# Kernel tuning notes

Measured on AMD Instinct MI355X. Metric: run time of the kernel, lower is better.

The kernel has to match this reference:

```python
import jax, jax.numpy as jnp
import numpy as np

N, C, H, K = 100000, 64, 8, 16
D = C // H  # head_dim = 8


def setup_inputs() -> dict:
    key = jax.random.key(0)
    ks = jax.random.split(key, 7)
    s = 1.0 / np.sqrt(C)
    return {
        "feats": jax.random.normal(ks[0], (N, C), jnp.float32),
        "knn_idx": jax.random.randint(ks[1], (N, K), 0, N, jnp.int32),
        "Wq": jax.random.normal(ks[2], (C, C), jnp.float32) * s,
        "Wk": jax.random.normal(ks[3], (C, C), jnp.float32) * s,
        "Wv": jax.random.normal(ks[4], (C, C), jnp.float32) * s,
        "Wo": jax.random.normal(ks[5], (C, C), jnp.float32) * s,
        "bo": jnp.zeros((C,), jnp.float32),
    }


def reference(feats, knn_idx, Wq, Wk, Wv, Wo, bo):
    # Projections (torch Linear y = x @ W^T expressed with pre-transposed W)
    q = (feats @ Wq).reshape(N, H, D)          # [N,H,D]
    k_feat = (feats @ Wk).reshape(N, H, D)     # [N,H,D]
    v = (feats @ Wv).reshape(N, H, D)          # [N,H,D]

    # Gather k-NN neighbors: [N,K,H,D]
    k_nb = k_feat[knn_idx]
    v_nb = v[knn_idx]

    # Scores: dot(q, k_neighbor) per head, scaled
    scores = jnp.einsum("nhd,nkhd->nkh", q, k_nb) / np.sqrt(D).astype(np.float32)
    attn = jax.nn.softmax(scores, axis=1)      # softmax over K neighbors

    out = jnp.einsum("nkh,nkhd->nhd", attn, v_nb).reshape(N, C)
    return out @ Wo + bo
```

## Files before the change

### kernel.cpp

```cpp
#include <hip/hip_runtime.h>
#include <hip/hip_fp16.h>
#include <math.h>

#define NPTS 100000
#define CDIM 64
#define KNN  16

typedef unsigned int uint;
typedef _Float16 f16x8 __attribute__((ext_vector_type(8)));
typedef _Float16 f16x2 __attribute__((ext_vector_type(2)));
typedef float    f32x4 __attribute__((ext_vector_type(4)));
typedef int      i32x4 __attribute__((ext_vector_type(4)));
typedef uint     u32x4 __attribute__((ext_vector_type(4)));
typedef uint     u32x2 __attribute__((ext_vector_type(2)));

template <int CTRL>
__device__ __forceinline__ float dpp_add_f(float x) {
    int yi = __builtin_amdgcn_mov_dpp(__float_as_int(x), CTRL, 0xF, 0xF, true);
    return x + __int_as_float(yi);
}

__device__ __forceinline__ float dot2acc(uint a, uint b, float c) {
#if __has_builtin(__builtin_amdgcn_fdot2)
    return __builtin_amdgcn_fdot2(__builtin_bit_cast(f16x2, a),
                                  __builtin_bit_cast(f16x2, b), c, false);
#else
    const f16x2 ha = __builtin_bit_cast(f16x2, a);
    const f16x2 hb = __builtin_bit_cast(f16x2, b);
    return c + (float)ha[0] * (float)hb[0] + (float)ha[1] * (float)hb[1];
#endif
}

__device__ __forceinline__ uint pkrtz(float a, float b) {
    union { __fp16 __attribute__((ext_vector_type(2))) h; uint u; } cv;
    cv.h = __builtin_amdgcn_cvt_pkrtz(a, b);
    return cv.u;
}


__global__ __launch_bounds__(256) void pack_w(
    const float* __restrict__ Wq, const float* __restrict__ Wk,
    const float* __restrict__ Wv, const float* __restrict__ Wo,
    __half* __restrict__ frag)
{
    const float* Ws[4] = {Wq, Wk, Wv, Wo};
    const float scale[4] = {0.3535533905932738f * 1.4426950408889634f, 1.f, 1.f, 1.f};
    f16x8* fp = (f16x8*)frag;
    const int e = blockIdx.x * 256 + threadIdx.x;
    const int lane = e & 63;
    const int ks   = (e >> 6) & 1;
    const int ct   = (e >> 7) & 3;
    const int mat  = e >> 9;
    const int m = lane & 15, quad = lane >> 4;
    const float* W = Ws[mat];
    const float sc = scale[mat];
    f16x8 b;
    #pragma unroll
    for (int j = 0; j < 8; ++j)
        b[j] = (_Float16)(sc * W[(size_t)(ks * 32 + quad * 8 + j) * 64 + ct * 16 + m]);
    fp[e] = b;
}

__device__ __forceinline__ f16x8 load_bfeat(const float* fp, int ks, int quad) {
    const float4 x0 = *(const float4*)(fp + ks * 32 + quad * 8);
    const float4 x1 = *(const float4*)(fp + ks * 32 + quad * 8 + 4);
    f16x8 a;
    a[0] = (_Float16)x0.x; a[1] = (_Float16)x0.y;
    a[2] = (_Float16)x0.z; a[3] = (_Float16)x0.w;
    a[4] = (_Float16)x1.x; a[5] = (_Float16)x1.y;
    a[6] = (_Float16)x1.z; a[7] = (_Float16)x1.w;
    return a;
}

__global__ __launch_bounds__(256) void proj_qkv(
    const float* __restrict__ feats, const __half* __restrict__ frag,
    __half* __restrict__ q, uint* __restrict__ kv)
{
    const int wid = blockIdx.x * 4 + (threadIdx.x >> 6);
    const int lane = threadIdx.x & 63;
    const int m = lane & 15, quad = lane >> 4;

    const f16x8* fp = (const f16x8*)frag;
    f16x8 Wf[3][4][2];
    #pragma unroll
    for (int mat = 0; mat < 3; ++mat)
        #pragma unroll
        for (int ct = 0; ct < 4; ++ct)
            #pragma unroll
            for (int ks = 0; ks < 2; ++ks)
                Wf[mat][ct][ks] = fp[((mat * 4 + ct) * 2 + ks) * 64 + lane];

    #pragma unroll
    for (int tt = 0; tt < 2; ++tt) {
        const int tile = wid * 2 + tt;
        if (tile >= NPTS / 16) break;
        const int r0 = tile * 16;
        const float* ap = feats + (size_t)(r0 + m) * 64;
        const f16x8 Bf0 = load_bfeat(ap, 0, quad);
        const f16x8 Bf1 = load_bfeat(ap, 1, quad);
        const size_t pt = (size_t)(r0 + m);

        #pragma unroll
        for (int ct = 0; ct < 4; ++ct) {
            f32x4 aq = {0.f, 0.f, 0.f, 0.f};
            f32x4 ak = {0.f, 0.f, 0.f, 0.f};
            f32x4 av = {0.f, 0.f, 0.f, 0.f};
            aq = __builtin_amdgcn_mfma_f32_16x16x32_f16(Wf[0][ct][0], Bf0, aq, 0, 0, 0);
            aq = __builtin_amdgcn_mfma_f32_16x16x32_f16(Wf[0][ct][1], Bf1, aq, 0, 0, 0);
            ak = __builtin_amdgcn_mfma_f32_16x16x32_f16(Wf[1][ct][0], Bf0, ak, 0, 0, 0);
            ak = __builtin_amdgcn_mfma_f32_16x16x32_f16(Wf[1][ct][1], Bf1, ak, 0, 0, 0);
            av = __builtin_amdgcn_mfma_f32_16x16x32_f16(Wf[2][ct][0], Bf0, av, 0, 0, 0);
            av = __builtin_amdgcn_mfma_f32_16x16x32_f16(Wf[2][ct][1], Bf1, av, 0, 0, 0);

            const int ch = ct * 16 + quad * 4;
            uint2 qp;
            qp.x = pkrtz(aq[0], aq[1]);
            qp.y = pkrtz(aq[2], aq[3]);
            *(uint2*)(q + pt * 64 + ch) = qp;
            uint4 kp;
            kp.x = pkrtz(ak[0], av[0]);
            kp.y = pkrtz(ak[1], av[1]);
            kp.z = pkrtz(ak[2], av[2]);
            kp.w = pkrtz(ak[3], av[3]);
            *(uint4*)(kv + pt * 64 + ch) = kp;
        }
    }
}

__global__ __launch_bounds__(256) void attn_out(
    const __half* __restrict__ q, const uint* __restrict__ kv,
    const int* __restrict__ knn, const __half* __restrict__ frag,
    const float* __restrict__ bo, float* __restrict__ out)
{
    __shared__ uint sO[16][36];
    const int t = threadIdx.x;
    const int lane = t & 63;
    const int w = t >> 6;
    const int l16 = lane & 15;
    const int p4 = lane >> 4;
    const int m = lane & 15, quad = lane >> 4;

    const int n0 = blockIdx.x * 16;
    const int n  = n0 + w * 4 + p4;

    const i32x4* kp = (const i32x4*)knn + (size_t)n * 4;
    const i32x4 i0 = __builtin_nontemporal_load(kp);
    const i32x4 i1 = __builtin_nontemporal_load(kp + 1);
    const i32x4 i2 = __builtin_nontemporal_load(kp + 2);
    const i32x4 i3 = __builtin_nontemporal_load(kp + 3);
    const int idx[KNN] = {i0[0], i0[1], i0[2], i0[3], i1[0], i1[1], i1[2], i1[3],
                          i2[0], i2[1], i2[2], i2[3], i3[0], i3[1], i3[2], i3[3]};

    const u32x2 qw = __builtin_nontemporal_load((const u32x2*)q + (size_t)n * 16 + l16);

    u32x4 u[KNN];
    #pragma unroll
    for (int i = 0; i < KNN; ++i)
        u[i] = *(const u32x4*)(kv + (size_t)idx[i] * 64 + 4 * l16);
    __builtin_amdgcn_sched_barrier(0);

    float ssum = 0.f;
    __half2 acc01 = __float2half2_rn(0.f);
    __half2 acc23 = __float2half2_rn(0.f);
    #pragma unroll
    for (int i = 0; i < KNN; ++i) {
        const uint kk01 = __builtin_amdgcn_perm(u[i][1], u[i][0], 0x05040100u);
        const uint kk23 = __builtin_amdgcn_perm(u[i][3], u[i][2], 0x05040100u);
        const uint vv01 = __builtin_amdgcn_perm(u[i][1], u[i][0], 0x07060302u);
        const uint vv23 = __builtin_amdgcn_perm(u[i][3], u[i][2], 0x07060302u);
        float s = dot2acc(qw[1], kk23, dot2acc(qw[0], kk01, 0.f));
        s = dpp_add_f<0xB1>(s);
        const float e = __builtin_amdgcn_exp2f(s);
        ssum += e;
        const __half2 w2 = __float2half2_rn(e);
        acc01 = __hfma2(w2, *(const __half2*)&vv01, acc01);
        acc23 = __hfma2(w2, *(const __half2*)&vv23, acc23);
    }

    const float inv = __builtin_amdgcn_rcpf(ssum);
    const __half2 iv = __float2half2_rn(inv);
    acc01 = __hmul2(acc01, iv);
    acc23 = __hmul2(acc23, iv);
    u32x2 ov;
    ov[0] = *(const uint*)&acc01;
    ov[1] = *(const uint*)&acc23;
    *(u32x2*)&sO[w * 4 + p4][2 * l16] = ov;
    __syncthreads();

    const f16x8* fpb = (const f16x8*)frag;
    const f16x8 Wf0 = fpb[((3 * 4 + w) * 2 + 0) * 64 + lane];
    const f16x8 Wf1 = fpb[((3 * 4 + w) * 2 + 1) * 64 + lane];

    const f16x8 Bf  = *(const f16x8*)&sO[m][quad * 4];
    const f16x8 Bf2 = *(const f16x8*)&sO[m][16 + quad * 4];
    f32x4 ac = {0.f, 0.f, 0.f, 0.f};
    ac = __builtin_amdgcn_mfma_f32_16x16x32_f16(Wf0, Bf, ac, 0, 0, 0);
    ac = __builtin_amdgcn_mfma_f32_16x16x32_f16(Wf1, Bf2, ac, 0, 0, 0);

    const int ch = w * 16 + quad * 4;
    const f32x4 bias = *(const f32x4*)(bo + ch);
    f32x4 o;
    o[0] = ac[0] + bias[0]; o[1] = ac[1] + bias[1];
    o[2] = ac[2] + bias[2]; o[3] = ac[3] + bias[3];
    __builtin_nontemporal_store(o, (f32x4*)(out + (size_t)(n0 + m) * 64 + ch));
}

extern "C" void kernel_launch(void* const* d_in, const int* in_sizes, int n_in,
                              void* d_out, int out_size, void* d_ws, size_t ws_size,
                              hipStream_t stream) {
    const float* feats = (const float*)d_in[0];
    const int*   knn   = (const int*)d_in[1];
    const float* Wq    = (const float*)d_in[2];
    const float* Wk    = (const float*)d_in[3];
    const float* Wv    = (const float*)d_in[4];
    const float* Wo    = (const float*)d_in[5];
    const float* bo    = (const float*)d_in[6];
    float* out = (float*)d_out;

    __half* frag = (__half*)d_ws;
    __half* q_h  = (__half*)((char*)d_ws + 32768);
    uint*   kvb  = (uint*)((char*)d_ws + 32768 +
                           (size_t)NPTS * CDIM * sizeof(__half));

    pack_w<<<8, 256, 0, stream>>>(Wq, Wk, Wv, Wo, frag);
    proj_qkv<<<782, 256, 0, stream>>>(feats, frag, q_h, kvb);
    attn_out<<<NPTS / 16, 256, 0, stream>>>(q_h, kvb, knn, frag, bo, out);
}
```

Measured before the change: 153.9 us.

## Fuse Q projection into attention kernel and batch neighbor gathers in halves

Removes the Q output from the projection kernel and recomputes Q per block inside the attention kernel via MFMA on feats, staging it through shared memory. This eliminates the fp16 q buffer write and read, at the cost of reading fp32 feats again and an extra block barrier before the gathers. The neighbor K/V gathers are also split into two batches of eight to reduce register pressure, possibly trading away some memory-level parallelism.

```diff
diff --git a/kernel.cpp b/kernel.cpp
--- a/kernel.cpp
+++ b/kernel.cpp
@@ -72,23 +72,23 @@
     return a;
 }
 
-__global__ __launch_bounds__(256) void proj_qkv(
+__global__ __launch_bounds__(256) void proj_kv(
     const float* __restrict__ feats, const __half* __restrict__ frag,
-    __half* __restrict__ q, uint* __restrict__ kv)
+    uint* __restrict__ kv)
 {
     const int wid = blockIdx.x * 4 + (threadIdx.x >> 6);
     const int lane = threadIdx.x & 63;
     const int m = lane & 15, quad = lane >> 4;
 
     const f16x8* fp = (const f16x8*)frag;
-    f16x8 Wf[3][4][2];
-    #pragma unroll
-    for (int mat = 0; mat < 3; ++mat)
+    f16x8 Wf[2][4][2];
+    #pragma unroll
+    for (int mat = 0; mat < 2; ++mat)
         #pragma unroll
         for (int ct = 0; ct < 4; ++ct)
             #pragma unroll
             for (int ks = 0; ks < 2; ++ks)
-                Wf[mat][ct][ks] = fp[((mat * 4 + ct) * 2 + ks) * 64 + lane];
+                Wf[mat][ct][ks] = fp[(((mat + 1) * 4 + ct) * 2 + ks) * 64 + lane];
 
     #pragma unroll
     for (int tt = 0; tt < 2; ++tt) {
@@ -102,21 +102,14 @@
 
         #pragma unroll
         for (int ct = 0; ct < 4; ++ct) {
-            f32x4 aq = {0.f, 0.f, 0.f, 0.f};
             f32x4 ak = {0.f, 0.f, 0.f, 0.f};
             f32x4 av = {0.f, 0.f, 0.f, 0.f};
-            aq = __builtin_amdgcn_mfma_f32_16x16x32_f16(Wf[0][ct][0], Bf0, aq, 0, 0, 0);
-            aq = __builtin_amdgcn_mfma_f32_16x16x32_f16(Wf[0][ct][1], Bf1, aq, 0, 0, 0);
-            ak = __builtin_amdgcn_mfma_f32_16x16x32_f16(Wf[1][ct][0], Bf0, ak, 0, 0, 0);
-            ak = __builtin_amdgcn_mfma_f32_16x16x32_f16(Wf[1][ct][1], Bf1, ak, 0, 0, 0);
-            av = __builtin_amdgcn_mfma_f32_16x16x32_f16(Wf[2][ct][0], Bf0, av, 0, 0, 0);
-            av = __builtin_amdgcn_mfma_f32_16x16x32_f16(Wf[2][ct][1], Bf1, av, 0, 0, 0);
+            ak = __builtin_amdgcn_mfma_f32_16x16x32_f16(Wf[0][ct][0], Bf0, ak, 0, 0, 0);
+            ak = __builtin_amdgcn_mfma_f32_16x16x32_f16(Wf[0][ct][1], Bf1, ak, 0, 0, 0);
+            av = __builtin_amdgcn_mfma_f32_16x16x32_f16(Wf[1][ct][0], Bf0, av, 0, 0, 0);
+            av = __builtin_amdgcn_mfma_f32_16x16x32_f16(Wf[1][ct][1], Bf1, av, 0, 0, 0);
 
             const int ch = ct * 16 + quad * 4;
-            uint2 qp;
-            qp.x = pkrtz(aq[0], aq[1]);
-            qp.y = pkrtz(aq[2], aq[3]);
-            *(uint2*)(q + pt * 64 + ch) = qp;
             uint4 kp;
             kp.x = pkrtz(ak[0], av[0]);
             kp.y = pkrtz(ak[1], av[1]);
@@ -128,10 +121,11 @@
 }
 
 __global__ __launch_bounds__(256) void attn_out(
-    const __half* __restrict__ q, const uint* __restrict__ kv,
+    const float* __restrict__ feats, const uint* __restrict__ kv,
     const int* __restrict__ knn, const __half* __restrict__ frag,
     const float* __restrict__ bo, float* __restrict__ out)
 {
+    __shared__ uint sQ[16][34];
     __shared__ uint sO[16][36];
     const int t = threadIdx.x;
     const int lane = t & 63;
@@ -151,30 +145,50 @@
     const int idx[KNN] = {i0[0], i0[1], i0[2], i0[3], i1[0], i1[1], i1[2], i1[3],
                           i2[0], i2[1], i2[2], i2[3], i3[0], i3[1], i3[2], i3[3]};
 
-    const u32x2 qw = __builtin_nontemporal_load((const u32x2*)q + (size_t)n * 16 + l16);
-
-    u32x4 u[KNN];
-    #pragma unroll
-    for (int i = 0; i < KNN; ++i)
-        u[i] = *(const u32x4*)(kv + (size_t)idx[i] * 64 + 4 * l16);
-    __builtin_amdgcn_sched_barrier(0);
+    const f16x8* fpb = (const f16x8*)frag;
+
+    {
+        const f16x8 WfQ0 = fpb[((0 * 4 + w) * 2 + 0) * 64 + lane];
+        const f16x8 WfQ1 = fpb[((0 * 4 + w) * 2 + 1) * 64 + lane];
+        const float* ap = feats + (size_t)(n0 + m) * 64;
+        const f16x8 Bf0 = load_bfeat(ap, 0, quad);
+        const f16x8 Bf1 = load_bfeat(ap, 1, quad);
+        f32x4 aq = {0.f, 0.f, 0.f, 0.f};
+        aq = __builtin_amdgcn_mfma_f32_16x16x32_f16(WfQ0, Bf0, aq, 0, 0, 0);
+        aq = __builtin_amdgcn_mfma_f32_16x16x32_f16(WfQ1, Bf1, aq, 0, 0, 0);
+        uint2 qp;
+        qp.x = pkrtz(aq[0], aq[1]);
+        qp.y = pkrtz(aq[2], aq[3]);
+        *(uint2*)&sQ[m][w * 8 + quad * 2] = qp;
+    }
+    __syncthreads();
+
+    const u32x2 qw = *(const u32x2*)&sQ[w * 4 + p4][2 * l16];
 
     float ssum = 0.f;
     __half2 acc01 = __float2half2_rn(0.f);
     __half2 acc23 = __float2half2_rn(0.f);
-    #pragma unroll
-    for (int i = 0; i < KNN; ++i) {
-        const uint kk01 = __builtin_amdgcn_perm(u[i][1], u[i][0], 0x05040100u);
-        const uint kk23 = __builtin_amdgcn_perm(u[i][3], u[i][2], 0x05040100u);
-        const uint vv01 = __builtin_amdgcn_perm(u[i][1], u[i][0], 0x07060302u);
-        const uint vv23 = __builtin_amdgcn_perm(u[i][3], u[i][2], 0x07060302u);
-        float s = dot2acc(qw[1], kk23, dot2acc(qw[0], kk01, 0.f));
-        s = dpp_add_f<0xB1>(s);
-        const float e = __builtin_amdgcn_exp2f(s);
-        ssum += e;
-        const __half2 w2 = __float2half2_rn(e);
-        acc01 = __hfma2(w2, *(const __half2*)&vv01, acc01);
-        acc23 = __hfma2(w2, *(const __half2*)&vv23, acc23);
+
+    #pragma unroll
+    for (int bb = 0; bb < 2; ++bb) {
+        u32x4 u[8];
+        #pragma unroll
+        for (int i = 0; i < 8; ++i)
+            u[i] = *(const u32x4*)(kv + (size_t)idx[bb * 8 + i] * 64 + 4 * l16);
+        #pragma unroll
+        for (int i = 0; i < 8; ++i) {
+            const uint kk01 = __builtin_amdgcn_perm(u[i][1], u[i][0], 0x05040100u);
+            const uint kk23 = __builtin_amdgcn_perm(u[i][3], u[i][2], 0x05040100u);
+            const uint vv01 = __builtin_amdgcn_perm(u[i][1], u[i][0], 0x07060302u);
+            const uint vv23 = __builtin_amdgcn_perm(u[i][3], u[i][2], 0x07060302u);
+            float s = dot2acc(qw[1], kk23, dot2acc(qw[0], kk01, 0.f));
+            s = dpp_add_f<0xB1>(s);
+            const float e = __builtin_amdgcn_exp2f(s);
+            ssum += e;
+            const __half2 w2 = __float2half2_rn(e);
+            acc01 = __hfma2(w2, *(const __half2*)&vv01, acc01);
+            acc23 = __hfma2(w2, *(const __half2*)&vv23, acc23);
+        }
     }
 
     const float inv = __builtin_amdgcn_rcpf(ssum);
@@ -187,7 +201,6 @@
     *(u32x2*)&sO[w * 4 + p4][2 * l16] = ov;
     __syncthreads();
 
-    const f16x8* fpb = (const f16x8*)frag;
     const f16x8 Wf0 = fpb[((3 * 4 + w) * 2 + 0) * 64 + lane];
     const f16x8 Wf1 = fpb[((3 * 4 + w) * 2 + 1) * 64 + lane];
 
@@ -218,11 +231,9 @@
     float* out = (float*)d_out;
 
     __half* frag = (__half*)d_ws;
-    __half* q_h  = (__half*)((char*)d_ws + 32768);
-    uint*   kvb  = (uint*)((char*)d_ws + 32768 +
-                           (size_t)NPTS * CDIM * sizeof(__half));
+    uint*   kvb  = (uint*)((char*)d_ws + 32768);
 
     pack_w<<<8, 256, 0, stream>>>(Wq, Wk, Wv, Wo, frag);
-    proj_qkv<<<782, 256, 0, stream>>>(feats, frag, q_h, kvb);
-    attn_out<<<NPTS / 16, 256, 0, stream>>>(q_h, kvb, knn, frag, bo, out);
-}
+    proj_kv<<<782, 256, 0, stream>>>(feats, frag, kvb);
+    attn_out<<<NPTS / 16, 256, 0, stream>>>(feats, kvb, knn, frag, bo, out);
+}
```

Result: no change. 155.2 us (+0.8%).
